# Kernel tuning notes

Hardware: AMD Instinct MI355X
Metric: run time of the kernel (lower is better)

Reference implementation:

```python
import jax, jax.numpy as jnp
from jax import lax
import numpy as np

B, T, D, H, O = 32, 2048, 256, 512, 256


def _lstm_layer(x_tbd, W_ih, W_hh, b_ih, b_hh):
    # x_tbd: [T, B, D_in]; W_ih: [4H, D_in]; W_hh: [4H, H]
    # PyTorch gate order: i, f, g, o
    xg = jnp.einsum('tbd,gd->tbg', x_tbd, W_ih) + b_ih + b_hh  # [T, B, 4H]
    h0 = jnp.zeros((x_tbd.shape[1], W_hh.shape[1]), x_tbd.dtype)
    c0 = jnp.zeros_like(h0)

    def step(carry, xg_t):
        h, c = carry
        g = xg_t + h @ W_hh.T  # [B, 4H]
        i, f, gg, o = jnp.split(g, 4, axis=-1)
        c = jax.nn.sigmoid(f) * c + jax.nn.sigmoid(i) * jnp.tanh(gg)
        h = jax.nn.sigmoid(o) * jnp.tanh(c)
        return (h, c), h

    (h_last, _), hs = lax.scan(step, (h0, c0), xg)
    return hs, h_last  # hs: [T, B, H]


def setup_inputs() -> dict:
    key = jax.random.key(0)
    ks = jax.random.split(key, 12)
    s = 1.0 / np.sqrt(H)  # PyTorch LSTM init scale
    inp = {
        'x': jax.random.normal(ks[0], (B, T, D), jnp.float32),
        'W_ih0': jax.random.uniform(ks[1], (4 * H, D), jnp.float32, -s, s),
        'W_hh0': jax.random.uniform(ks[2], (4 * H, H), jnp.float32, -s, s),
        'b_ih0': jax.random.uniform(ks[3], (4 * H,), jnp.float32, -s, s),
        'b_hh0': jax.random.uniform(ks[4], (4 * H,), jnp.float32, -s, s),
        'W_ih1': jax.random.uniform(ks[5], (4 * H, H), jnp.float32, -s, s),
        'W_hh1': jax.random.uniform(ks[6], (4 * H, H), jnp.float32, -s, s),
        'b_ih1': jax.random.uniform(ks[7], (4 * H,), jnp.float32, -s, s),
        'b_hh1': jax.random.uniform(ks[8], (4 * H,), jnp.float32, -s, s),
        'W_out': jax.random.uniform(ks[9], (O, H), jnp.float32, -s, s),
        'b_out': jax.random.uniform(ks[10], (O,), jnp.float32, -s, s),
    }
    return inp


def reference(x, W_ih0, W_hh0, b_ih0, b_hh0, W_ih1, W_hh1, b_ih1, b_hh1, W_out, b_out):
    x_tbd = jnp.transpose(x, (1, 0, 2))  # batch_first -> time major
    hs0, _ = _lstm_layer(x_tbd, W_ih0, W_hh0, b_ih0, b_hh0)
    _, h1_last = _lstm_layer(hs0, W_ih1, W_hh1, b_ih1, b_hh1)
    # out = Linear(hidden[0][-1]) : final hidden state of layer 2
    return h1_last @ W_out.T + b_out  # [B, O]
```

## Files before the change

kernel.cpp:

```cpp
#include <hip/hip_runtime.h>
#include <hip/hip_bf16.h>

#define TT 2048
#define BB 32
#define DD 256
#define HH 512
#define NWG 32
#define UPW 16

using f32x4 = __attribute__((ext_vector_type(4))) float;
using s16x8 = __attribute__((ext_vector_type(8))) short;

__device__ __attribute__((aligned(16))) __hip_bfloat16 g_h0[TT + 1][BB][HH];
__device__ __attribute__((aligned(16))) __hip_bfloat16 g_h1[TT + 1][BB][HH];
__device__ __attribute__((aligned(16))) float g_h1f[BB][HH];
__device__ int g_flag0[TT + 1][NWG];
__device__ int g_flag1[TT + 1][NWG];

__device__ __forceinline__ short f2bf(float f) {
    union { float f; unsigned u; } v; v.f = f;
    unsigned r = v.u + 0x7fffu + ((v.u >> 16) & 1u);
    return (short)(r >> 16);
}
__device__ __forceinline__ float sigm(float x) { return 1.f / (1.f + __expf(-x)); }
__device__ __forceinline__ float tanh_f(float x) { return 1.f - 2.f / (__expf(2.f * x) + 1.f); }

__device__ __forceinline__ s16x8 aload16(const __hip_bfloat16* p) {
    const unsigned long long* q = (const unsigned long long*)p;
    union { unsigned long long u[2]; s16x8 v; } r;
    r.u[0] = __hip_atomic_load(q,     __ATOMIC_RELAXED, __HIP_MEMORY_SCOPE_AGENT);
    r.u[1] = __hip_atomic_load(q + 1, __ATOMIC_RELAXED, __HIP_MEMORY_SCOPE_AGENT);
    return r.v;
}

template <int LAYER>
__device__ void scan_layer(char* smem, int wgk,
                           const float* __restrict__ Wih, const float* __restrict__ Whh,
                           const float* __restrict__ bih, const float* __restrict__ bhh,
                           const float* __restrict__ x) {
    constexpr int KIN = (LAYER == 0) ? DD : HH;
    constexpr int KL  = KIN + HH;
    constexpr int QK  = KL / 4;
    constexpr int NKQ = QK / 32;
    constexpr int NGR = KL / 128;
    constexpr int ROWB = 2048;

    const int tid  = threadIdx.x;
    const int wave = tid >> 6;
    const int lane = tid & 63;
    const int m    = wave & 1;
    const int q    = wave >> 1;
    const int u16  = lane & 15;
    const int hi   = lane >> 4;

    s16x8 wreg[NKQ * 4];
    {
        const int unit = wgk * UPW + u16;
#pragma unroll
        for (int ks = 0; ks < NKQ; ++ks) {
#pragma unroll
            for (int gt = 0; gt < 4; ++gt) {
                const int k = q * QK + ks * 32 + hi * 8;
                const float* src = (k < KIN)
                    ? (Wih + (size_t)(gt * HH + unit) * KIN + k)
                    : (Whh + (size_t)(gt * HH + unit) * HH + (k - KIN));
                s16x8 w;
#pragma unroll
                for (int j = 0; j < 8; ++j) w[j] = f2bf(src[j]);
                wreg[ks * 4 + gt] = w;
            }
        }
    }

    const int eb = tid >> 4;
    const int eu = tid & 15;
    const int unit_g = wgk * UPW + eu;
    float bias[4];
#pragma unroll
    for (int gt = 0; gt < 4; ++gt)
        bias[gt] = bih[gt * HH + unit_g] + bhh[gt * HH + unit_g];
    float c = 0.f;

    float* gbuf = (float*)smem;

    for (int t = 0; t < TT; ++t) {
        s16x8 xpre[2];
        if (LAYER == 0) {
            const int b = tid >> 4;
#pragma unroll
            for (int g = 0; g < 2; ++g) {
                const int k = ((tid & 15) + 16 * g) * 8;
                const float* xs = x + ((size_t)b * TT + t) * DD + k;
                const float4 x0 = *(const float4*)xs;
                const float4 x1 = *(const float4*)(xs + 4);
                s16x8 v;
                v[0] = f2bf(x0.x); v[1] = f2bf(x0.y); v[2] = f2bf(x0.z); v[3] = f2bf(x0.w);
                v[4] = f2bf(x1.x); v[5] = f2bf(x1.y); v[6] = f2bf(x1.z); v[7] = f2bf(x1.w);
                xpre[g] = v;
            }
        }

        if (wave == 0) {
            int iters = 0;
            for (;;) {
                int v;
                if (LAYER == 0) {
                    v = (lane < NWG)
                        ? __hip_atomic_load(&g_flag0[t][lane], __ATOMIC_RELAXED, __HIP_MEMORY_SCOPE_AGENT)
                        : 1;
                } else {
                    v = (lane < NWG)
                        ? __hip_atomic_load(&g_flag0[t + 1][lane], __ATOMIC_RELAXED, __HIP_MEMORY_SCOPE_AGENT)
                        : __hip_atomic_load(&g_flag1[t][lane - NWG], __ATOMIC_RELAXED, __HIP_MEMORY_SCOPE_AGENT);
                }
                if (__all(v != 0)) break;
                if (++iters > (1 << 22)) break;
            }
        }
        __syncthreads();

        {
            const int b = tid >> 4;
#pragma unroll
            for (int g = 0; g < NGR; ++g) {
                const int kg = (tid & 15) + 16 * g;
                const int k  = kg * 8;
                s16x8 v;
                if (LAYER == 0) {
                    if (g < 2) v = xpre[g];
                    else       v = aload16(&g_h0[t][b][k - KIN]);
                } else {
                    if (g < 4) v = aload16(&g_h0[t + 1][b][k]);
                    else       v = aload16(&g_h1[t][b][k - KIN]);
                }
                const int off = kg * 16;
                *(s16x8*)(smem + b * ROWB + (off ^ ((b & 7) << 4))) = v;
            }
        }
        __syncthreads();

        f32x4 acc[4] = {{0,0,0,0},{0,0,0,0},{0,0,0,0},{0,0,0,0}};
        {
            const int arow = m * 16 + u16;
            const char* abase = smem + arow * ROWB;
            const int aswz = (arow & 7) << 4;
#pragma unroll
            for (int ks = 0; ks < NKQ; ++ks) {
                const int off = (q * QK + ks * 32 + hi * 8) * 2;
                s16x8 a = *(const s16x8*)(abase + (off ^ aswz));
#pragma unroll
                for (int gt = 0; gt < 4; ++gt)
                    acc[gt] = __builtin_amdgcn_mfma_f32_16x16x32_bf16(a, wreg[ks * 4 + gt], acc[gt], 0, 0, 0);
            }
        }
        __syncthreads();

#pragma unroll
        for (int gt = 0; gt < 4; ++gt) {
#pragma unroll
            for (int r = 0; r < 4; ++r) {
                const int b = m * 16 + hi * 4 + r;
                gbuf[(q * BB + b) * 68 + gt * 16 + u16] = acc[gt][r];
            }
        }
        __syncthreads();

        {
            float gv[4];
#pragma unroll
            for (int gt = 0; gt < 4; ++gt) {
                float s = bias[gt];
#pragma unroll
                for (int qq = 0; qq < 4; ++qq) s += gbuf[(qq * BB + eb) * 68 + gt * 16 + eu];
                gv[gt] = s;
            }
            const float ig = sigm(gv[0]);
            const float fg = sigm(gv[1]);
            const float gg = tanh_f(gv[2]);
            const float og = sigm(gv[3]);
            c = fg * c + ig * gg;
            const float h = og * tanh_f(c);
            const unsigned hu = (unsigned)(unsigned short)f2bf(h);
            const unsigned other = __shfl_xor(hu, 1);
            if (LAYER == 1 && t == TT - 1) g_h1f[eb][unit_g] = h;
            if ((eu & 1) == 0) {
                const unsigned packed = hu | (other << 16);
                unsigned* dst = (LAYER == 0)
                    ? (unsigned*)&g_h0[t + 1][eb][unit_g]
                    : (unsigned*)&g_h1[t + 1][eb][unit_g];
                __hip_atomic_store(dst, packed, __ATOMIC_RELAXED, __HIP_MEMORY_SCOPE_AGENT);
            }
        }
        asm volatile("s_waitcnt vmcnt(0)" ::: "memory");
        __syncthreads();
        if (tid == 0) {
            if (LAYER == 0)
                __hip_atomic_store(&g_flag0[t + 1][wgk], 1, __ATOMIC_RELAXED, __HIP_MEMORY_SCOPE_AGENT);
            else
                __hip_atomic_store(&g_flag1[t + 1][wgk], 1, __ATOMIC_RELAXED, __HIP_MEMORY_SCOPE_AGENT);
        }
    }
}

__global__ __launch_bounds__(512, 2) void lstm_scan(
    const float* __restrict__ x,
    const float* __restrict__ Wih0, const float* __restrict__ Whh0,
    const float* __restrict__ bih0, const float* __restrict__ bhh0,
    const float* __restrict__ Wih1, const float* __restrict__ Whh1,
    const float* __restrict__ bih1, const float* __restrict__ bhh1) {
    __shared__ __attribute__((aligned(16))) char smem[65536];
    const int layer = blockIdx.x >> 5;
    const int wgk   = blockIdx.x & (NWG - 1);
    if (layer == 0) scan_layer<0>(smem, wgk, Wih0, Whh0, bih0, bhh0, x);
    else            scan_layer<1>(smem, wgk, Wih1, Whh1, bih1, bhh1, nullptr);
}

__global__ void reset_kernel() {
    const int n = (TT + 1) * NWG;
    int* f0 = &g_flag0[0][0];
    int* f1 = &g_flag1[0][0];
    for (int i = blockIdx.x * blockDim.x + threadIdx.x; i < n; i += gridDim.x * blockDim.x) {
        const int v = (i < NWG) ? 1 : 0;
        f0[i] = v;
        f1[i] = v;
    }
    unsigned short* h0 = (unsigned short*)&g_h0[0][0][0];
    unsigned short* h1 = (unsigned short*)&g_h1[0][0][0];
    for (int i = blockIdx.x * blockDim.x + threadIdx.x; i < BB * HH; i += gridDim.x * blockDim.x) {
        h0[i] = 0;
        h1[i] = 0;
    }
}

__global__ void out_kernel(const float* __restrict__ Wout, const float* __restrict__ bout,
                           float* __restrict__ out) {
    const int b = blockIdx.x;
    const int o = threadIdx.x;
    const float4* h4 = (const float4*)&g_h1f[b][0];
    const float4* w4 = (const float4*)(Wout + (size_t)o * HH);
    float s = bout[o];
    for (int k = 0; k < HH / 4; ++k) {
        const float4 a = h4[k], w = w4[k];
        s += a.x * w.x + a.y * w.y + a.z * w.z + a.w * w.w;
    }
    out[b * 256 + o] = s;
}

extern "C" void kernel_launch(void* const* d_in, const int* in_sizes, int n_in,
                              void* d_out, int out_size, void* d_ws, size_t ws_size,
                              hipStream_t stream) {
    const float* x    = (const float*)d_in[0];
    const float* Wih0 = (const float*)d_in[1];
    const float* Whh0 = (const float*)d_in[2];
    const float* bih0 = (const float*)d_in[3];
    const float* bhh0 = (const float*)d_in[4];
    const float* Wih1 = (const float*)d_in[5];
    const float* Whh1 = (const float*)d_in[6];
    const float* bih1 = (const float*)d_in[7];
    const float* bhh1 = (const float*)d_in[8];
    const float* Wout = (const float*)d_in[9];
    const float* bout = (const float*)d_in[10];
    float* out = (float*)d_out;

    hipLaunchKernelGGL(reset_kernel, dim3(128), dim3(256), 0, stream);
    hipLaunchKernelGGL(lstm_scan, dim3(2 * NWG), dim3(512), 0, stream,
                       x, Wih0, Whh0, bih0, bhh0, Wih1, Whh1, bih1, bhh1);
    hipLaunchKernelGGL(out_kernel, dim3(BB), dim3(256), 0, stream, Wout, bout, out);
}
```

Measured before the change: 11.20 ms.

## Replace per-step flag barriers with sequence-tagged ring buffer of hidden states

Hidden-state exchange between workgroups now uses a 64-slot ring of 64-bit words, each carrying packed bf16 data plus a step tag. Consumers poll the data words directly instead of waiting on separate per-workgroup flags. This removes the flag round trip, the vmcnt wait and two block barriers per step. The input x is pre-converted to bf16 in a prep kernel, and a separate gate buffer in shared memory lets one syncthreads be dropped. A progress counter throttles layer 0 so it cannot overrun the ring. The risks are extra polling traffic and the ring depth limiting how far layer 0 can run ahead.

New measurement: 13.39 ms. +19.5%, slower.

```diff
diff --git a/kernel.cpp b/kernel.cpp
--- a/kernel.cpp
+++ b/kernel.cpp
@@ -7,15 +7,18 @@
 #define HH 512
 #define NWG 32
 #define UPW 16
-
+#define RING 64
+
+typedef unsigned long long u64;
+typedef unsigned u32;
 using f32x4 = __attribute__((ext_vector_type(4))) float;
 using s16x8 = __attribute__((ext_vector_type(8))) short;
 
-__device__ __attribute__((aligned(16))) __hip_bfloat16 g_h0[TT + 1][BB][HH];
-__device__ __attribute__((aligned(16))) __hip_bfloat16 g_h1[TT + 1][BB][HH];
+__device__ __attribute__((aligned(16))) u64 g_r0[RING][BB][HH / 2];
+__device__ __attribute__((aligned(16))) u64 g_r1[RING][BB][HH / 2];
+__device__ __attribute__((aligned(16))) __hip_bfloat16 g_xb[BB][TT][DD];
 __device__ __attribute__((aligned(16))) float g_h1f[BB][HH];
-__device__ int g_flag0[TT + 1][NWG];
-__device__ int g_flag1[TT + 1][NWG];
+__device__ int g_prog1;
 
 __device__ __forceinline__ short f2bf(float f) {
     union { float f; unsigned u; } v; v.f = f;
@@ -25,24 +28,17 @@
 __device__ __forceinline__ float sigm(float x) { return 1.f / (1.f + __expf(-x)); }
 __device__ __forceinline__ float tanh_f(float x) { return 1.f - 2.f / (__expf(2.f * x) + 1.f); }
 
-__device__ __forceinline__ s16x8 aload16(const __hip_bfloat16* p) {
-    const unsigned long long* q = (const unsigned long long*)p;
-    union { unsigned long long u[2]; s16x8 v; } r;
-    r.u[0] = __hip_atomic_load(q,     __ATOMIC_RELAXED, __HIP_MEMORY_SCOPE_AGENT);
-    r.u[1] = __hip_atomic_load(q + 1, __ATOMIC_RELAXED, __HIP_MEMORY_SCOPE_AGENT);
-    return r.v;
-}
-
 template <int LAYER>
 __device__ void scan_layer(char* smem, int wgk,
                            const float* __restrict__ Wih, const float* __restrict__ Whh,
-                           const float* __restrict__ bih, const float* __restrict__ bhh,
-                           const float* __restrict__ x) {
+                           const float* __restrict__ bih, const float* __restrict__ bhh) {
     constexpr int KIN = (LAYER == 0) ? DD : HH;
     constexpr int KL  = KIN + HH;
     constexpr int QK  = KL / 4;
     constexpr int NKQ = QK / 32;
     constexpr int NGR = KL / 128;
+    constexpr int NXG = (LAYER == 0) ? 2 : 0;
+    constexpr int NHG = NGR - NXG;
     constexpr int ROWB = 2048;
 
     const int tid  = threadIdx.x;
@@ -50,12 +46,12 @@
     const int lane = tid & 63;
     const int m    = wave & 1;
     const int q    = wave >> 1;
-    const int u16  = lane & 15;
+    const int u16i = lane & 15;
     const int hi   = lane >> 4;
 
     s16x8 wreg[NKQ * 4];
     {
-        const int unit = wgk * UPW + u16;
+        const int unit = wgk * UPW + u16i;
 #pragma unroll
         for (int ks = 0; ks < NKQ; ++ks) {
 #pragma unroll
@@ -81,67 +77,86 @@
         bias[gt] = bih[gt * HH + unit_g] + bhh[gt * HH + unit_g];
     float c = 0.f;
 
-    float* gbuf = (float*)smem;
+    const int sb = tid >> 4;
+    const int sk = tid & 15;
+
+    float* gbuf = (float*)(smem + 65536);
 
     for (int t = 0; t < TT; ++t) {
-        s16x8 xpre[2];
+        if (LAYER == 0 && (t & 15) == 0) {
+            int it = 0;
+            while (__hip_atomic_load(&g_prog1, __ATOMIC_RELAXED, __HIP_MEMORY_SCOPE_AGENT) < t - 32) {
+                if (++it > (1 << 20)) break;
+            }
+        }
+
         if (LAYER == 0) {
-            const int b = tid >> 4;
-#pragma unroll
-            for (int g = 0; g < 2; ++g) {
-                const int k = ((tid & 15) + 16 * g) * 8;
-                const float* xs = x + ((size_t)b * TT + t) * DD + k;
-                const float4 x0 = *(const float4*)xs;
-                const float4 x1 = *(const float4*)(xs + 4);
-                s16x8 v;
-                v[0] = f2bf(x0.x); v[1] = f2bf(x0.y); v[2] = f2bf(x0.z); v[3] = f2bf(x0.w);
-                v[4] = f2bf(x1.x); v[5] = f2bf(x1.y); v[6] = f2bf(x1.z); v[7] = f2bf(x1.w);
-                xpre[g] = v;
-            }
-        }
-
-        if (wave == 0) {
-            int iters = 0;
+#pragma unroll
+            for (int g = 0; g < NXG; ++g) {
+                const int kg = sk + 16 * g;
+                s16x8 v = *(const s16x8*)&g_xb[sb][t][kg * 8];
+                *(s16x8*)(smem + sb * ROWB + ((kg * 16) ^ ((sb & 7) << 4))) = v;
+            }
+        }
+
+        u64 hw[NHG][4];
+        const u64* hp[NHG];
+        u32 expv[NHG];
+#pragma unroll
+        for (int g = 0; g < NHG; ++g) {
+            const int k = (sk + 16 * (g + NXG)) * 8;
+            if (LAYER == 0) {
+                hp[g] = &g_r0[t & (RING - 1)][sb][(k - DD) / 2];
+                expv[g] = (u32)t;
+            } else if (g < 4) {
+                hp[g] = &g_r0[(t + 1) & (RING - 1)][sb][k / 2];
+                expv[g] = (u32)(t + 1);
+            } else {
+                hp[g] = &g_r1[t & (RING - 1)][sb][(k - HH) / 2];
+                expv[g] = (u32)t;
+            }
+        }
+#pragma unroll
+        for (int g = 0; g < NHG; ++g)
+#pragma unroll
+            for (int j = 0; j < 4; ++j)
+                hw[g][j] = __hip_atomic_load(hp[g] + j, __ATOMIC_RELAXED, __HIP_MEMORY_SCOPE_AGENT);
+        {
+            int it = 0;
             for (;;) {
-                int v;
-                if (LAYER == 0) {
-                    v = (lane < NWG)
-                        ? __hip_atomic_load(&g_flag0[t][lane], __ATOMIC_RELAXED, __HIP_MEMORY_SCOPE_AGENT)
-                        : 1;
-                } else {
-                    v = (lane < NWG)
-                        ? __hip_atomic_load(&g_flag0[t + 1][lane], __ATOMIC_RELAXED, __HIP_MEMORY_SCOPE_AGENT)
-                        : __hip_atomic_load(&g_flag1[t][lane - NWG], __ATOMIC_RELAXED, __HIP_MEMORY_SCOPE_AGENT);
-                }
-                if (__all(v != 0)) break;
-                if (++iters > (1 << 22)) break;
-            }
-        }
-        __syncthreads();
-
-        {
-            const int b = tid >> 4;
-#pragma unroll
-            for (int g = 0; g < NGR; ++g) {
-                const int kg = (tid & 15) + 16 * g;
-                const int k  = kg * 8;
-                s16x8 v;
-                if (LAYER == 0) {
-                    if (g < 2) v = xpre[g];
-                    else       v = aload16(&g_h0[t][b][k - KIN]);
-                } else {
-                    if (g < 4) v = aload16(&g_h0[t + 1][b][k]);
-                    else       v = aload16(&g_h1[t][b][k - KIN]);
-                }
-                const int off = kg * 16;
-                *(s16x8*)(smem + b * ROWB + (off ^ ((b & 7) << 4))) = v;
-            }
-        }
+                u32 bad = 0;
+#pragma unroll
+                for (int g = 0; g < NHG; ++g)
+#pragma unroll
+                    for (int j = 0; j < 4; ++j)
+                        if ((u32)(hw[g][j] >> 32) != expv[g]) bad |= (1u << (g * 4 + j));
+                if (!bad) break;
+                if (++it > (1 << 15)) break;
+#pragma unroll
+                for (int g = 0; g < NHG; ++g)
+#pragma unroll
+                    for (int j = 0; j < 4; ++j)
+                        if (bad & (1u << (g * 4 + j)))
+                            hw[g][j] = __hip_atomic_load(hp[g] + j, __ATOMIC_RELAXED, __HIP_MEMORY_SCOPE_AGENT);
+            }
+        }
+#pragma unroll
+        for (int g = 0; g < NHG; ++g) {
+            const int kg = sk + 16 * (g + NXG);
+            s16x8 v;
+#pragma unroll
+            for (int j = 0; j < 4; ++j) {
+                v[2 * j]     = (short)(u32)hw[g][j];
+                v[2 * j + 1] = (short)((u32)hw[g][j] >> 16);
+            }
+            *(s16x8*)(smem + sb * ROWB + ((kg * 16) ^ ((sb & 7) << 4))) = v;
+        }
+
         __syncthreads();
 
         f32x4 acc[4] = {{0,0,0,0},{0,0,0,0},{0,0,0,0},{0,0,0,0}};
         {
-            const int arow = m * 16 + u16;
+            const int arow = m * 16 + u16i;
             const char* abase = smem + arow * ROWB;
             const int aswz = (arow & 7) << 4;
 #pragma unroll
@@ -153,16 +168,16 @@
                     acc[gt] = __builtin_amdgcn_mfma_f32_16x16x32_bf16(a, wreg[ks * 4 + gt], acc[gt], 0, 0, 0);
             }
         }
-        __syncthreads();
 
 #pragma unroll
         for (int gt = 0; gt < 4; ++gt) {
 #pragma unroll
             for (int r = 0; r < 4; ++r) {
                 const int b = m * 16 + hi * 4 + r;
-                gbuf[(q * BB + b) * 68 + gt * 16 + u16] = acc[gt][r];
-            }
-        }
+                gbuf[(q * BB + b) * 68 + gt * 16 + u16i] = acc[gt][r];
+            }
+        }
+
         __syncthreads();
 
         {
@@ -180,55 +195,52 @@
             const float og = sigm(gv[3]);
             c = fg * c + ig * gg;
             const float h = og * tanh_f(c);
-            const unsigned hu = (unsigned)(unsigned short)f2bf(h);
-            const unsigned other = __shfl_xor(hu, 1);
+            const u32 hu = (u32)(unsigned short)f2bf(h);
+            const u32 other = __shfl_xor(hu, 1);
             if (LAYER == 1 && t == TT - 1) g_h1f[eb][unit_g] = h;
             if ((eu & 1) == 0) {
-                const unsigned packed = hu | (other << 16);
-                unsigned* dst = (LAYER == 0)
-                    ? (unsigned*)&g_h0[t + 1][eb][unit_g]
-                    : (unsigned*)&g_h1[t + 1][eb][unit_g];
-                __hip_atomic_store(dst, packed, __ATOMIC_RELAXED, __HIP_MEMORY_SCOPE_AGENT);
-            }
-        }
-        asm volatile("s_waitcnt vmcnt(0)" ::: "memory");
-        __syncthreads();
-        if (tid == 0) {
-            if (LAYER == 0)
-                __hip_atomic_store(&g_flag0[t + 1][wgk], 1, __ATOMIC_RELAXED, __HIP_MEMORY_SCOPE_AGENT);
-            else
-                __hip_atomic_store(&g_flag1[t + 1][wgk], 1, __ATOMIC_RELAXED, __HIP_MEMORY_SCOPE_AGENT);
+                const u64 w = (u64)(hu | (other << 16)) | ((u64)(u32)(t + 1) << 32);
+                u64* dst = (LAYER == 0)
+                    ? &g_r0[(t + 1) & (RING - 1)][eb][unit_g / 2]
+                    : &g_r1[(t + 1) & (RING - 1)][eb][unit_g / 2];
+                __hip_atomic_store(dst, w, __ATOMIC_RELAXED, __HIP_MEMORY_SCOPE_AGENT);
+            }
+            if (LAYER == 1 && wgk == 0 && tid == 0)
+                __hip_atomic_store(&g_prog1, t + 1, __ATOMIC_RELAXED, __HIP_MEMORY_SCOPE_AGENT);
         }
     }
 }
 
 __global__ __launch_bounds__(512, 2) void lstm_scan(
-    const float* __restrict__ x,
     const float* __restrict__ Wih0, const float* __restrict__ Whh0,
     const float* __restrict__ bih0, const float* __restrict__ bhh0,
     const float* __restrict__ Wih1, const float* __restrict__ Whh1,
     const float* __restrict__ bih1, const float* __restrict__ bhh1) {
-    __shared__ __attribute__((aligned(16))) char smem[65536];
+    __shared__ __attribute__((aligned(16))) char smem[65536 + 4 * BB * 68 * 4];
     const int layer = blockIdx.x >> 5;
     const int wgk   = blockIdx.x & (NWG - 1);
-    if (layer == 0) scan_layer<0>(smem, wgk, Wih0, Whh0, bih0, bhh0, x);
-    else            scan_layer<1>(smem, wgk, Wih1, Whh1, bih1, bhh1, nullptr);
-}
-
-__global__ void reset_kernel() {
-    const int n = (TT + 1) * NWG;
-    int* f0 = &g_flag0[0][0];
-    int* f1 = &g_flag1[0][0];
-    for (int i = blockIdx.x * blockDim.x + threadIdx.x; i < n; i += gridDim.x * blockDim.x) {
-        const int v = (i < NWG) ? 1 : 0;
-        f0[i] = v;
-        f1[i] = v;
-    }
-    unsigned short* h0 = (unsigned short*)&g_h0[0][0][0];
-    unsigned short* h1 = (unsigned short*)&g_h1[0][0][0];
-    for (int i = blockIdx.x * blockDim.x + threadIdx.x; i < BB * HH; i += gridDim.x * blockDim.x) {
-        h0[i] = 0;
-        h1[i] = 0;
+    if (layer == 0) scan_layer<0>(smem, wgk, Wih0, Whh0, bih0, bhh0);
+    else            scan_layer<1>(smem, wgk, Wih1, Whh1, bih1, bhh1);
+}
+
+__global__ void prep_kernel(const float* __restrict__ x) {
+    const int wg = blockIdx.x;
+    const int tid = threadIdx.x;
+    if (wg < 64) {
+        ulonglong2* base = (ulonglong2*)((wg < 32) ? &g_r0[0][0][0] : &g_r1[0][0][0]);
+        const int per = (RING * BB * (HH / 2)) / 2 / 32;
+        ulonglong2* p = base + (size_t)(wg & 31) * per;
+        const ulonglong2 z = {0ull, 0ull};
+        for (int i = tid; i < per; i += 256) p[i] = z;
+        if (wg == 0 && tid == 0) g_prog1 = 0;
+    } else {
+        const size_t i = (size_t)(wg - 64) * 256 + tid;
+        const float4* xs = (const float4*)x + i * 2;
+        const float4 a = xs[0], b = xs[1];
+        s16x8 v;
+        v[0] = f2bf(a.x); v[1] = f2bf(a.y); v[2] = f2bf(a.z); v[3] = f2bf(a.w);
+        v[4] = f2bf(b.x); v[5] = f2bf(b.y); v[6] = f2bf(b.z); v[7] = f2bf(b.w);
+        ((s16x8*)&g_xb[0][0][0])[i] = v;
     }
 }
 
@@ -262,8 +274,8 @@
     const float* bout = (const float*)d_in[10];
     float* out = (float*)d_out;
 
-    hipLaunchKernelGGL(reset_kernel, dim3(128), dim3(256), 0, stream);
+    hipLaunchKernelGGL(prep_kernel, dim3(64 + 8192), dim3(256), 0, stream, x);
     hipLaunchKernelGGL(lstm_scan, dim3(2 * NWG), dim3(512), 0, stream,
-                       x, Wih0, Whh0, bih0, bhh0, Wih1, Whh1, bih1, bhh1);
+                       Wih0, Whh0, bih0, bhh0, Wih1, Whh1, bih1, bhh1);
     hipLaunchKernelGGL(out_kernel, dim3(BB), dim3(256), 0, stream, Wout, bout, out);
 }
```
